# Performance work log

Hardware: AMD Instinct MI355X
Metric: run time of the kernel (lower is better)

The kernel has to match this reference:

```python
import jax, jax.numpy as jnp
import numpy as np

B = 32; H = 56; W = 56; C = 384; NH = 12; WS = 14; SS = 7
L = H * W; N = WS * WS; HD = C // NH; SCALE = HD ** -0.5; HID = 4 * C
NW = (H // WS) * (W // WS)
EPS = 1e-5

def _relative_index():
    ch = np.arange(WS)[:, None].repeat(WS, 1)
    cw = np.arange(WS)[None, :].repeat(WS, 0)
    coords = np.stack([ch, cw], -1).reshape(-1, 2)  # [N,2]
    rel = coords[:, None, :] - coords[None, :, :]
    rel = rel + (WS - 1)
    rel[:, :, 0] *= 2 * WS - 1
    return rel.sum(-1)  # [N,N], values in [0,(2WS-1)^2)

def _attn_mask():
    img = np.zeros((H, W))
    sl = (slice(0, -WS), slice(-WS, -SS), slice(-SS, None))
    cnt = 0
    for hs in sl:
        for ws_ in sl:
            img[hs, ws_] = cnt; cnt += 1
    mw = img.reshape(H // WS, WS, W // WS, WS).transpose(0, 2, 1, 3).reshape(-1, N)
    am = mw[:, None, :] - mw[:, :, None]  # [nW,N,N]
    return np.where(am != 0, -100.0, 0.0).astype(np.float32)

REL_IDX = jnp.asarray(_relative_index())
MASK = jnp.asarray(_attn_mask())  # [NW,N,N]

def _ln(x, w, b):
    m = jnp.mean(x, -1, keepdims=True)
    v = jnp.mean((x - m) ** 2, -1, keepdims=True)
    return (x - m) * jax.lax.rsqrt(v + EPS) * w + b

def setup_inputs() -> dict:
    key = jax.random.key(0)
    ks = jax.random.split(key, 8)
    s = 0.02
    return {
        "x": jax.random.normal(ks[0], (B, L, C), jnp.float32),
        "norm1_w": jnp.ones((C,), jnp.float32),
        "norm1_b": jnp.zeros((C,), jnp.float32),
        "qkv_w": jax.random.normal(ks[1], (3 * C, C), jnp.float32) * s,
        "qkv_b": jnp.zeros((3 * C,), jnp.float32),
        "proj_w": jax.random.normal(ks[2], (C, C), jnp.float32) * s,
        "proj_b": jnp.zeros((C,), jnp.float32),
        "relative_table": jax.random.normal(ks[3], ((2 * WS - 1) ** 2, 2 * NH), jnp.float32) * s,
        "norm2_w": jnp.ones((C,), jnp.float32),
        "norm2_b": jnp.zeros((C,), jnp.float32),
        "fc1_w": jax.random.normal(ks[4], (HID, C), jnp.float32) * s,
        "fc1_b": jnp.zeros((HID,), jnp.float32),
        "fc2_w": jax.random.normal(ks[5], (C, HID), jnp.float32) * s,
        "fc2_b": jnp.zeros((C,), jnp.float32),
    }

def reference(x, norm1_w, norm1_b, qkv_w, qkv_b, proj_w, proj_b,
              relative_table, norm2_w, norm2_b, fc1_w, fc1_b, fc2_w, fc2_b):
    shortcut = x
    xn = _ln(x, norm1_w, norm1_b).reshape(B, H, W, C)
    # cyclic shift + window partition -> [B*NW, N, C]
    xs = jnp.roll(xn, (-SS, -SS), (1, 2))
    xw = xs.reshape(B, H // WS, WS, W // WS, WS, C).transpose(0, 1, 3, 2, 4, 5).reshape(-1, N, C)
    B_ = B * NW
    qkv = (xw @ qkv_w.T + qkv_b).reshape(B_, N, 3, NH, HD).transpose(2, 0, 3, 1, 4)
    q, k, v = qkv[0] * SCALE, qkv[1], qkv[2]  # [B_,NH,N,HD]
    attn = jnp.einsum('bhnd,bhmd->bhnm', q, k)  # [B_,NH,N,N]
    rel = relative_table[REL_IDX]  # [N,N,2*NH]
    rel = rel.transpose(2, 0, 1)  # [2*NH,N,N]
    bias, rscale = rel[:NH], rel[NH:]
    attn = attn + bias[None]
    attn = attn.reshape(B, NW, NH, N, N) + MASK[None, :, None]
    attn = jax.nn.softmax(attn.reshape(B_, NH, N, N), axis=-1)
    attn = attn * rscale[None]  # multiplicative relative scale AFTER softmax
    out = jnp.einsum('bhnm,bhmd->bhnd', attn, v)
    out = out.transpose(0, 2, 1, 3).reshape(B_, N, C)
    out = out @ proj_w.T + proj_b
    # window reverse + reverse shift
    xr = out.reshape(B, H // WS, W // WS, WS, WS, C).transpose(0, 1, 3, 2, 4, 5).reshape(B, H, W, C)
    xr = jnp.roll(xr, (SS, SS), (1, 2)).reshape(B, L, C)
    x = shortcut + xr
    h = _ln(x, norm2_w, norm2_b)
    h = jax.nn.gelu(h @ fc1_w.T + fc1_b, approximate=False) @ fc2_w.T + fc2_b
    return x + h
```

## Files before the change

kernel.cpp:

```cpp
#include <hip/hip_runtime.h>
#include <hip/hip_bf16.h>
#include <math.h>

#define BDIM 32
#define HDIM 56
#define WDIM 56
#define CDIM 384
#define NHEAD 12
#define WSZ 14
#define SSZ 7
#define LDIM (HDIM*WDIM)
#define NTOK (WSZ*WSZ)
#define HDHEAD (CDIM/NHEAD)
#define HIDDIM (4*CDIM)
#define NWIN 16
#define BWIN (BDIM*NWIN)
#define MROWS (BDIM*LDIM)
#define EPSLN 1e-5f
#define ATTSCALE 0.17677669529663687f

#define KROW 40
#define VROW 232
#define PROW 232

typedef __hip_bfloat16 bf16;
typedef __attribute__((ext_vector_type(8))) short bf16x8;
typedef __attribute__((ext_vector_type(4))) short s16x4;
typedef __attribute__((ext_vector_type(4))) float f32x4;

#define ASYNC16(gp, lp) __builtin_amdgcn_global_load_lds( \
    (__attribute__((address_space(1))) void*)(gp),        \
    (__attribute__((address_space(3))) void*)(lp), 16, 0, 0)

static __device__ __forceinline__ short f2bfs(float x) {
  union { bf16 h; short s; } u; u.h = __float2bfloat16(x); return u.s;
}
static __device__ __forceinline__ float bfs2f(short s) {
  unsigned int u = ((unsigned int)(unsigned short)s) << 16;
  float f; __builtin_memcpy(&f, &u, 4); return f;
}
static __device__ __forceinline__ float tof(float x) { return x; }
static __device__ __forceinline__ float tof(bf16 x)  { return __bfloat162float(x); }

__global__ __launch_bounds__(256) void k_cvt(const float* __restrict__ in,
                                             bf16* __restrict__ out, int n)
{
  int i = blockIdx.x * 256 + threadIdx.x;
  if (i < n) out[i] = __float2bfloat16(in[i]);
}

template<bool WIN, typename TIN>
__global__ __launch_bounds__(128) void k_ln(const TIN* __restrict__ xin,
    const float* __restrict__ gw, const float* __restrict__ gb,
    bf16* __restrict__ out)
{
  int r = blockIdx.x;
  int t = threadIdx.x;
  const TIN* xp = xin + (size_t)r * CDIM;
  float v0 = tof(xp[t]), v1 = tof(xp[t+128]), v2 = tof(xp[t+256]);
  float s  = v0+v1+v2;
  float ss = v0*v0 + v1*v1 + v2*v2;
  #pragma unroll
  for (int o = 32; o > 0; o >>= 1) { s += __shfl_down(s, o); ss += __shfl_down(ss, o); }
  __shared__ float red[4];
  if ((t & 63) == 0) { red[(t>>6)*2] = s; red[(t>>6)*2+1] = ss; }
  __syncthreads();
  float mean = (red[0]+red[2]) * (1.0f/CDIM);
  float var  = (red[1]+red[3]) * (1.0f/CDIM) - mean*mean;
  float rstd = rsqrtf(var + EPSLN);

  size_t orow;
  if (WIN) {
    int b = r / LDIM, l = r % LDIM;
    int h = l / WDIM, w = l % WDIM;
    int h2 = (h + HDIM - SSZ) % HDIM, w2 = (w + WDIM - SSZ) % WDIM;
    int wh = h2 / WSZ, ii = h2 % WSZ, ww = w2 / WSZ, jj = w2 % WSZ;
    int b_ = b*NWIN + wh*4 + ww;
    int n  = ii*WSZ + jj;
    orow = ((size_t)b_*NTOK + n) * CDIM;
  } else {
    orow = (size_t)r * CDIM;
  }
  out[orow+t]     = __float2bfloat16((v0-mean)*rstd*gw[t]     + gb[t]);
  out[orow+t+128] = __float2bfloat16((v1-mean)*rstd*gw[t+128] + gb[t+128]);
  out[orow+t+256] = __float2bfloat16((v2-mean)*rstd*gw[t+256] + gb[t+256]);
}

template<int KD, int EPI>
__global__ __launch_bounds__(256) void k_mgemm(
    const bf16* __restrict__ A, const bf16* __restrict__ Wb,
    const float* __restrict__ bias, const float* __restrict__ aux,
    const bf16* __restrict__ auxb,
    float* __restrict__ outf, bf16* __restrict__ outb, int gx)
{
  __shared__ short As[2][128*32];
  __shared__ short Bs[2][128*32];
  int tid  = threadIdx.x;
  int lane = tid & 63, wid = tid >> 6;
  int c15 = lane & 15, h4 = lane >> 4;
  int wr = wid >> 1, wc = wid & 1;

  int nwg = gridDim.x, bid = blockIdx.x;
  int swz = (bid & 7) * (nwg >> 3) + (bid >> 3);
  int ty = swz / gx, tx = swz - ty * gx;
  int row0 = ty * 128, col0 = tx * 128;

  f32x4 acc[4][4] = {};

  int srow[2];
  int skk = (lane & 3) * 8;
  #pragma unroll
  for (int s = 0; s < 2; s++) {
    int c = wid*2 + s;
    srow[s] = c*16 + (lane >> 2);
  }

  for (int k0 = 0; k0 < KD; k0 += 64) {
    #pragma unroll
    for (int s = 0; s < 2; s++) {
      int c = wid*2 + s;
      const bf16* ap = A  + (size_t)(row0 + srow[s])*KD + k0 + skk;
      const bf16* bp = Wb + (size_t)(col0 + srow[s])*KD + k0 + skk;
      ASYNC16(ap,      &As[0][c*512]);
      ASYNC16(bp,      &Bs[0][c*512]);
      ASYNC16(ap + 32, &As[1][c*512]);
      ASYNC16(bp + 32, &Bs[1][c*512]);
    }
    __syncthreads();

    #pragma unroll
    for (int half = 0; half < 2; half++) {
      bf16x8 af[4], bfr[4];
      #pragma unroll
      for (int m = 0; m < 4; m++)
        af[m] = *reinterpret_cast<const bf16x8*>(
            &As[half][(wr*64 + m*16 + c15)*32 + h4*8]);
      #pragma unroll
      for (int n = 0; n < 4; n++)
        bfr[n] = *reinterpret_cast<const bf16x8*>(
            &Bs[half][(wc*64 + n*16 + c15)*32 + h4*8]);
      #pragma unroll
      for (int n = 0; n < 4; n++)
        #pragma unroll
        for (int m = 0; m < 4; m++)
          acc[n][m] = __builtin_amdgcn_mfma_f32_16x16x32_bf16(bfr[n], af[m], acc[n][m], 0, 0, 0);
    }
    __syncthreads();
  }

  int rb = row0 + wr*64 + c15;
  int cb = col0 + wc*64 + h4*4;
  #pragma unroll
  for (int m = 0; m < 4; m++) {
    int r = rb + m*16;
    if constexpr (EPI == 0) {
      int b_ = r / NTOK, nn = r % NTOK;
      const size_t QKVSTRIDE = (size_t)BWIN*NHEAD*NTOK*HDHEAD;
      #pragma unroll
      for (int n = 0; n < 4; n++) {
        int c0 = cb + n*16;
        f32x4 v = acc[n][m];
        f32x4 b4 = *(const f32x4*)&bias[c0];
        int which = c0 / CDIM, rem = c0 - which*CDIM;
        int hh = rem >> 5, dd = rem & 31;
        float scl = (which == 0) ? ATTSCALE : 1.f;
        s16x4 o;
        #pragma unroll
        for (int i = 0; i < 4; i++) o[i] = f2bfs((v[i] + b4[i]) * scl);
        *(s16x4*)&outb[(size_t)which*QKVSTRIDE + (((size_t)b_*NHEAD+hh)*NTOK+nn)*HDHEAD + dd] = o;
      }
    } else if constexpr (EPI == 1) {
      int b_ = r / NTOK, nn = r % NTOK;
      int b = b_ >> 4, wi = b_ & 15, wh = wi >> 2, ww = wi & 3;
      int ii = nn / WSZ, jj = nn % WSZ;
      int hh = (wh*WSZ + ii + SSZ) % HDIM;
      int wcc = (ww*WSZ + jj + SSZ) % WDIM;
      size_t rr = ((size_t)b*LDIM + hh*WDIM + wcc) * CDIM;
      #pragma unroll
      for (int n = 0; n < 4; n++) {
        int c0 = cb + n*16;
        f32x4 v = acc[n][m];
        f32x4 b4 = *(const f32x4*)&bias[c0];
        f32x4 a4 = *(const f32x4*)&aux[rr + c0];
        s16x4 o;
        #pragma unroll
        for (int i = 0; i < 4; i++) o[i] = f2bfs(a4[i] + v[i] + b4[i]);
        *(s16x4*)&outb[rr + c0] = o;
      }
    } else if constexpr (EPI == 2) {
      #pragma unroll
      for (int n = 0; n < 4; n++) {
        int c0 = cb + n*16;
        f32x4 v = acc[n][m];
        f32x4 b4 = *(const f32x4*)&bias[c0];
        s16x4 o;
        #pragma unroll
        for (int i = 0; i < 4; i++) {
          float val = v[i] + b4[i];
          val = 0.5f * val * (1.0f + erff(val * 0.70710678118654752f));
          o[i] = f2bfs(val);
        }
        *(s16x4*)&outb[(size_t)r*HIDDIM + c0] = o;
      }
    } else {
      #pragma unroll
      for (int n = 0; n < 4; n++) {
        int c0 = cb + n*16;
        f32x4 v = acc[n][m];
        f32x4 b4 = *(const f32x4*)&bias[c0];
        s16x4 ab = *(const s16x4*)&auxb[(size_t)r*CDIM + c0];
        f32x4 o;
        #pragma unroll
        for (int i = 0; i < 4; i++) o[i] = v[i] + b4[i] + bfs2f(ab[i]);
        *(f32x4*)&outf[(size_t)r*CDIM + c0] = o;
      }
    }
  }
}

__global__ __launch_bounds__(256) void k_attn_mfma(const bf16* __restrict__ q,
    const bf16* __restrict__ k, const bf16* __restrict__ v,
    const float* __restrict__ rt, bf16* __restrict__ out)
{
  __shared__ short  Ks[208*KROW];
  __shared__ short  Vt[32*VROW];
  __shared__ short  Ps[4][16*PROW];
  __shared__ float2 tab2[729];
  __shared__ int    regv[208];

  int blk = blockIdx.x;
  int b_ = blk / NHEAD, head = blk % NHEAD;
  int tid = threadIdx.x, lane = tid & 63, wid = tid >> 6;
  int c15 = lane & 15, h4 = lane >> 4;

  const bf16* kp = k + (size_t)blk*NTOK*HDHEAD;
  const bf16* vp = v + (size_t)blk*NTOK*HDHEAD;
  for (int c = tid; c < 784; c += 256) {
    int m = c >> 2, k8 = (c & 3) * 8;
    *(bf16x8*)&Ks[m*KROW + k8] = *(const bf16x8*)(kp + m*32 + k8);
    bf16x8 vv = *(const bf16x8*)(vp + m*32 + k8);
    #pragma unroll
    for (int j = 0; j < 8; j++) Vt[(k8+j)*VROW + m] = vv[j];
  }
  for (int e = tid; e < 12*KROW; e += 256) Ks[196*KROW + e] = 0;
  for (int e = tid; e < 32*28; e += 256) Vt[(e/28)*VROW + 196 + (e%28)] = 0;
  for (int e = tid; e < 729; e += 256)
    tab2[e] = make_float2(rt[e*2*NHEAD + head], rt[e*2*NHEAD + NHEAD + head]);
  {
    int wi = b_ & 15, wh = wi >> 2, ww = wi & 3;
    for (int e = tid; e < 208; e += 256) {
      int rv = 0;
      if (e < NTOK) {
        int i = e / WSZ, j = e % WSZ;
        int ha = wh*WSZ + i, wa = ww*WSZ + j;
        int rh = ha < (HDIM-WSZ) ? 0 : (ha < (HDIM-SSZ) ? 1 : 2);
        int rw = wa < (WDIM-WSZ) ? 0 : (wa < (WDIM-SSZ) ? 1 : 2);
        rv = rh*3 + rw;
      }
      regv[e] = rv;
    }
  }
  __syncthreads();

  int   moff[13], mreg[13];
  float mpad[13];
  #pragma unroll
  for (int t = 0; t < 13; t++) {
    int m  = t*16 + c15;
    int mm = min(m, NTOK-1);
    moff[t] = (mm/WSZ)*27 + (mm%WSZ);
    mreg[t] = regv[mm];
    mpad[t] = (m >= NTOK) ? -1e30f : 0.f;
  }

  short* myP = &Ps[wid][0];
  #pragma unroll
  for (int i = 0; i < 4; i++) myP[(h4*4+i)*PROW + 208 + c15] = 0;

  bf16* op = out + (size_t)b_*NTOK*CDIM + head*HDHEAD;

  for (int t4 = 0; t4 < 4; t4++) {
    int s = t4*4 + wid;
    if (s < 13) {
      int qrow = min(s*16 + c15, NTOK-1);
      bf16x8 qf = *(const bf16x8*)(q + ((size_t)blk*NTOK + qrow)*HDHEAD + h4*8);

      f32x4 sc[13];
      #pragma unroll
      for (int t = 0; t < 13; t++) {
        bf16x8 kf = *(const bf16x8*)&Ks[(t*16 + c15)*KROW + h4*8];
        sc[t] = __builtin_amdgcn_mfma_f32_16x16x32_bf16(qf, kf, (f32x4){0.f,0.f,0.f,0.f}, 0, 0, 0);
      }

      #pragma unroll
      for (int i = 0; i < 4; i++) {
        int n  = s*16 + h4*4 + i;
        int nc = min(n, NTOK-1);
        int nbase = ((nc/WSZ) + 13)*27 + (nc%WSZ) + 13;
        int nreg  = regv[nc];
        float rr[13];
        float sum = 0.f;
        #pragma unroll
        for (int t = 0; t < 13; t++) {
          float2 hr = tab2[nbase - moff[t]];
          float sv = sc[t][i] + hr.x + ((mreg[t] != nreg) ? -100.f : 0.f) + mpad[t];
          float e = __expf(sv);
          rr[t] = hr.y;
          sc[t][i] = e; sum += e;
        }
        #pragma unroll
        for (int o = 1; o < 16; o <<= 1) sum += __shfl_xor(sum, o);
        float inv = 1.f / sum;
        int prow = h4*4 + i;
        #pragma unroll
        for (int t = 0; t < 13; t++)
          myP[prow*PROW + t*16 + c15] = f2bfs(sc[t][i] * inv * rr[t]);
      }
    }

    __syncthreads();

    if (s < 13) {
      f32x4 o0 = {0.f,0.f,0.f,0.f}, o1 = {0.f,0.f,0.f,0.f};
      #pragma unroll
      for (int t7 = 0; t7 < 7; t7++) {
        bf16x8 pf = *(const bf16x8*)&myP[c15*PROW + t7*32 + h4*8];
        bf16x8 v0 = *(const bf16x8*)&Vt[c15*VROW + t7*32 + h4*8];
        bf16x8 v1 = *(const bf16x8*)&Vt[(16 + c15)*VROW + t7*32 + h4*8];
        o0 = __builtin_amdgcn_mfma_f32_16x16x32_bf16(pf, v0, o0, 0, 0, 0);
        o1 = __builtin_amdgcn_mfma_f32_16x16x32_bf16(pf, v1, o1, 0, 0, 0);
      }

      #pragma unroll
      for (int i = 0; i < 4; i++) {
        int n = s*16 + h4*4 + i;
        if (n < NTOK) {
          op[(size_t)n*CDIM + c15]      = __float2bfloat16(o0[i]);
          op[(size_t)n*CDIM + 16 + c15] = __float2bfloat16(o1[i]);
        }
      }
    }

    __syncthreads();
  }
}

extern "C" void kernel_launch(void* const* d_in, const int* in_sizes, int n_in,
                              void* d_out, int out_size, void* d_ws, size_t ws_size,
                              hipStream_t stream)
{
  const float* x      = (const float*)d_in[0];
  const float* n1w    = (const float*)d_in[1];
  const float* n1b    = (const float*)d_in[2];
  const float* qkv_w  = (const float*)d_in[3];
  const float* qkv_b  = (const float*)d_in[4];
  const float* proj_w = (const float*)d_in[5];
  const float* proj_b = (const float*)d_in[6];
  const float* rt     = (const float*)d_in[7];
  const float* n2w    = (const float*)d_in[8];
  const float* n2b    = (const float*)d_in[9];
  const float* fc1_w  = (const float*)d_in[10];
  const float* fc1_b  = (const float*)d_in[11];
  const float* fc2_w  = (const float*)d_in[12];
  const float* fc2_b  = (const float*)d_in[13];

  char* ws = (char*)d_ws;
  const size_t SZ_BF = (size_t)MROWS * CDIM * 2;
  bf16*  xw      = (bf16*)ws;
  bf16*  attnout = (bf16*)ws;
  bf16*  qkv     = (bf16*)(ws + SZ_BF);
  bf16*  x2b     = (bf16*)(ws + SZ_BF);
  bf16*  hln     = (bf16*)(ws + 2*SZ_BF);
  bf16*  hid     = (bf16*)(ws + 4*SZ_BF);
  const int NQKVW = 3*CDIM*CDIM;
  const int NPROJW = CDIM*CDIM;
  const int NFCW  = HIDDIM*CDIM;
  bf16* wq  = (bf16*)(ws + 4*SZ_BF);
  bf16* wp  = wq + NQKVW;
  bf16* wf1 = (bf16*)ws;
  bf16* wf2 = wf1 + NFCW;
  const size_t QKVSTRIDE = (size_t)BWIN*NHEAD*NTOK*HDHEAD;

  k_cvt<<<(NQKVW+255)/256, 256, 0, stream>>>(qkv_w, wq, NQKVW);
  k_cvt<<<(NPROJW+255)/256, 256, 0, stream>>>(proj_w, wp, NPROJW);

  k_ln<true, float><<<MROWS, 128, 0, stream>>>(x, n1w, n1b, xw);
  k_mgemm<CDIM, 0><<<9*(MROWS/128), 256, 0, stream>>>(
      xw, wq, qkv_b, nullptr, nullptr, nullptr, qkv, 9);
  k_attn_mfma<<<BWIN*NHEAD, 256, 0, stream>>>(
      qkv, qkv + QKVSTRIDE, qkv + 2*QKVSTRIDE, rt, attnout);
  k_mgemm<CDIM, 1><<<3*(MROWS/128), 256, 0, stream>>>(
      attnout, wp, proj_b, x, nullptr, nullptr, x2b, 3);

  k_cvt<<<(NFCW+255)/256, 256, 0, stream>>>(fc1_w, wf1, NFCW);
  k_cvt<<<(NFCW+255)/256, 256, 0, stream>>>(fc2_w, wf2, NFCW);

  k_ln<false, bf16><<<MROWS, 128, 0, stream>>>(x2b, n2w, n2b, hln);
  k_mgemm<CDIM, 2><<<12*(MROWS/128), 256, 0, stream>>>(
      hln, wf1, fc1_b, nullptr, nullptr, nullptr, hid, 12);
  k_mgemm<HIDDIM, 3><<<3*(MROWS/128), 256, 0, stream>>>(
      hid, wf2, fc2_b, nullptr, x2b, (float*)d_out, nullptr, 3);
}
```

Baseline: 1.087 ms.

## Double-buffer GEMM K-tiles with prefetch and XOR-swizzled LDS layout

Reworks the bf16 MFMA GEMM main loop so the next 64-wide K tile is loaded asynchronously into a second LDS buffer while the current tile is computed. The loop previously loaded, synced and computed in sequence. The LDS tile layout also changes from two 32-wide halves to a single 64-wide row with an XOR swizzle on 16-byte chunks, to reduce bank conflicts on the fragment reads. LDS usage doubles to 64KB per block, which may lower occupancy. The visible loop also lacks a barrier between compute and the next overwrite, so correctness depends on sync code that is not shown.

```diff
diff --git a/kernel.cpp b/kernel.cpp
--- a/kernel.cpp
+++ b/kernel.cpp
@@ -93,8 +93,8 @@
     const bf16* __restrict__ auxb,
     float* __restrict__ outf, bf16* __restrict__ outb, int gx)
 {
-  __shared__ short As[2][128*32];
-  __shared__ short Bs[2][128*32];
+  __shared__ short As[2][128*64];
+  __shared__ short Bs[2][128*64];
   int tid  = threadIdx.x;
   int lane = tid & 63, wid = tid >> 6;
   int c15 = lane & 15, h4 = lane >> 4;
@@ -107,38 +107,44 @@
 
   f32x4 acc[4][4] = {};
 
-  int srow[2];
-  int skk = (lane & 3) * 8;
+  int srow = lane >> 3;
+  int skk  = ((lane & 7) ^ srow) * 8;
+
+  const int NT = KD / 64;
+
   #pragma unroll
-  for (int s = 0; s < 2; s++) {
-    int c = wid*2 + s;
-    srow[s] = c*16 + (lane >> 2);
-  }
-
-  for (int k0 = 0; k0 < KD; k0 += 64) {
-    #pragma unroll
-    for (int s = 0; s < 2; s++) {
-      int c = wid*2 + s;
-      const bf16* ap = A  + (size_t)(row0 + srow[s])*KD + k0 + skk;
-      const bf16* bp = Wb + (size_t)(col0 + srow[s])*KD + k0 + skk;
-      ASYNC16(ap,      &As[0][c*512]);
-      ASYNC16(bp,      &Bs[0][c*512]);
-      ASYNC16(ap + 32, &As[1][c*512]);
-      ASYNC16(bp + 32, &Bs[1][c*512]);
-    }
-    __syncthreads();
-
+  for (int s = 0; s < 4; s++) {
+    int c = wid*4 + s;
+    ASYNC16(A  + (size_t)(row0 + c*8 + srow)*KD + skk, &As[0][c*512]);
+    ASYNC16(Wb + (size_t)(col0 + c*8 + srow)*KD + skk, &Bs[0][c*512]);
+  }
+  __syncthreads();
+
+  for (int t = 0; t < NT; t++) {
+    int cur = t & 1;
+    if (t + 1 < NT) {
+      int k1 = (t+1)*64;
+      #pragma unroll
+      for (int s = 0; s < 4; s++) {
+        int c = wid*4 + s;
+        ASYNC16(A  + (size_t)(row0 + c*8 + srow)*KD + k1 + skk, &As[cur^1][c*512]);
+        ASYNC16(Wb + (size_t)(col0 + c*8 + srow)*KD + k1 + skk, &Bs[cur^1][c*512]);
+      }
+    }
     #pragma unroll
     for (int half = 0; half < 2; half++) {
       bf16x8 af[4], bfr[4];
-      #pragma unroll
-      for (int m = 0; m < 4; m++)
-        af[m] = *reinterpret_cast<const bf16x8*>(
-            &As[half][(wr*64 + m*16 + c15)*32 + h4*8]);
-      #pragma unroll
-      for (int n = 0; n < 4; n++)
-        bfr[n] = *reinterpret_cast<const bf16x8*>(
-            &Bs[half][(wc*64 + n*16 + c15)*32 + h4*8]);
+      int blk8 = ((half << 2) + h4) ^ (c15 & 7);
+      #pragma unroll
+      for (int m = 0; m < 4; m++) {
+        int rr = wr*64 + m*16 + c15;
+        af[m] = *reinterpret_cast<const bf16x8*>(&As[cur][rr*64 + blk8*8]);
+      }
+      #pragma unroll
+      for (int n = 0; n < 4; n++) {
+        int rr = wc*64 + n*16 + c15;
+        bfr[n] = *reinterpret_cast<const bf16x8*>(&Bs[cur][rr*64 + blk8*8]);
+      }
       #pragma unroll
       for (int n = 0; n < 4; n++)
         #pragma unroll
```

New measurement: 1.116 ms. 2.7% more time.
